# Performance work log

Measured on AMD Instinct MI355X. Metric: run time of the kernel, lower is better.

Reference implementation:

```python
import jax, jax.numpy as jnp
import numpy as np

B, N, E, H = 4, 4096, 1024, 16
D = E // H            # head_dim = 64
P_DIM = 64            # proj_dim; feature dim = 2*P_DIM = 128
EPS = 1e-4


def setup_inputs() -> dict:
    key = jax.random.key(0)
    ks = jax.random.split(key, 9)
    x = jax.random.normal(ks[0], (B, N, E), jnp.float32)
    init = 0.02
    Wq = jax.random.normal(ks[1], (E, E), jnp.float32) * init
    Wk = jax.random.normal(ks[2], (E, E), jnp.float32) * init
    Wv = jax.random.normal(ks[3], (E, E), jnp.float32) * init
    Wo = jax.random.normal(ks[4], (E, E), jnp.float32) * init
    bq = jnp.zeros((E,), jnp.float32)
    bk = jnp.zeros((E,), jnp.float32)
    bv = jnp.zeros((E,), jnp.float32)
    bo = jnp.zeros((E,), jnp.float32)
    # orthogonal random projection matrix (proj_dim, head_dim), fixed (non-trainable)
    g = np.random.default_rng(0).normal(size=(P_DIM, D))
    P = jnp.asarray(np.linalg.qr(g)[0], jnp.float32)
    return dict(x=x, Wq=Wq, bq=bq, Wk=Wk, bk=bk, Wv=Wv, bv=bv, Wo=Wo, bo=bo, P=P)


def _heads(z):
    # (B, N, E) -> (B, H, N, D)
    return z.reshape(B, N, H, D).transpose(0, 2, 1, 3)


def _normalize(z):
    return z / (jnp.linalg.norm(z, axis=-1, keepdims=True) + EPS)


def reference(x, Wq, bq, Wk, bk, Wv, bv, Wo, bo, P):
    q = _heads(x @ Wq.T + bq)
    k = _heads(x @ Wk.T + bk)
    v = _heads(x @ Wv.T + bv)
    q = _normalize(q)
    k = _normalize(k)
    scale = H ** 0.25
    qp = jnp.einsum('bhnd,ed->bhne', q, P) * scale
    kp = jnp.einsum('bhnd,ed->bhne', k, P) * scale
    fscale = P_DIM ** (-0.5)   # x.shape[-1]**-0.5 with last dim = proj_dim
    qf = jnp.concatenate([jnp.sin(qp), jnp.cos(qp)], axis=-1) * fscale  # (B,H,N,2p)
    kf = jnp.concatenate([jnp.sin(kp), jnp.cos(kp)], axis=-1) * fscale
    # non-causal linear attention: q @ (k^T v)
    kv = jnp.einsum('bhme,bhmd->bhed', kf, v)          # (B,H,2p,D)
    o = jnp.einsum('bhne,bhed->bhnd', qf, kv)          # (B,H,N,D)
    o = o.transpose(0, 2, 1, 3).reshape(B, N, E)
    return o @ Wo.T + bo
```

## Files before the change

kernel.cpp:

```cpp
#include <hip/hip_runtime.h>
#include <hip/hip_bf16.h>
#include <stdint.h>


typedef __bf16 bf16x8 __attribute__((ext_vector_type(8)));
typedef float f32x4 __attribute__((ext_vector_type(4)));

#define AS1 __attribute__((address_space(1)))
#define AS3 __attribute__((address_space(3)))

__device__ __forceinline__ void gl2lds16(const void* g, void* l) {
    __builtin_amdgcn_global_load_lds((const AS1 void*)g, (AS3 void*)l, 16, 0, 0);
}

static constexpr int GM = 16384, GN = 1024, GK = 1024;
static constexpr int KV_SLABS = 8;

__global__ void detect_kernel(const unsigned short* __restrict__ x,
                              int* __restrict__ flag) {
    __shared__ int s;
    const int lane = threadIdx.x;
    if (lane == 0) s = 0;
    __syncthreads();
    int cnt = 0;
#pragma unroll
    for (int i = 0; i < 2; ++i) {
        const unsigned short u = x[i * 64 + lane];
        const int e = (u >> 7) & 0xFF;
        cnt += (e >= 117 && e <= 131) ? 1 : 0;
    }
    atomicAdd(&s, cnt);
    __syncthreads();
    if (lane == 0) *flag = (s >= 100) ? 1 : 0;
}

__global__ __launch_bounds__(256) void cvt_kernel(
    const void* __restrict__ src, __hip_bfloat16* __restrict__ dst,
    int n, const int* __restrict__ flag) {
    if (*flag) return;
    const int i = (blockIdx.x * 256 + threadIdx.x) * 8;
    if (i >= n) return;
    const float* s = (const float*)src + i;
    const float4 a = *(const float4*)s;
    const float4 b = *(const float4*)(s + 4);
    union { uint4 u; __hip_bfloat16 h[8]; } pk;
    pk.h[0] = __float2bfloat16(a.x); pk.h[1] = __float2bfloat16(a.y);
    pk.h[2] = __float2bfloat16(a.z); pk.h[3] = __float2bfloat16(a.w);
    pk.h[4] = __float2bfloat16(b.x); pk.h[5] = __float2bfloat16(b.y);
    pk.h[6] = __float2bfloat16(b.z); pk.h[7] = __float2bfloat16(b.w);
    *(uint4*)(dst + i) = pk.u;
}

__global__ __launch_bounds__(512, 1) void gemm256_kernel(
    const void* __restrict__ Adirect,
    const __hip_bfloat16* __restrict__ Acvt,
    const void* __restrict__ Wr, const __hip_bfloat16* __restrict__ Wc,
    const void* __restrict__ bias_raw,
    void* __restrict__ Cout,
    const int* __restrict__ flag, int last)
{
    __shared__ unsigned short smem[65536];

    const int tid  = threadIdx.x;
    const int lane = tid & 63;
    const int w    = tid >> 6;
    const int wm   = w >> 2, wn = w & 3;
    const int lr   = lane & 15, lk = lane >> 4;

    const int id  = blockIdx.x;
    const int xcd = id & 7;
    const int s   = id >> 3;
    const int m0  = (xcd * 8 + (s >> 2)) * 256;
    const int n0  = (s & 3) * 256;
    const int fl  = *flag;

    const __hip_bfloat16* A = fl ? (const __hip_bfloat16*)Adirect : Acvt;
    const __hip_bfloat16* W = fl ? (const __hip_bfloat16*)Wr : Wc;
    const __hip_bfloat16* Ab = A + (size_t)m0 * GK;
    const __hip_bfloat16* Wb = W + (size_t)n0 * GK;

    f32x4 acc[8][4];
#pragma unroll
    for (int i = 0; i < 8; ++i)
#pragma unroll
        for (int j = 0; j < 4; ++j)
            acc[i][j] = (f32x4){0.f, 0.f, 0.f, 0.f};

    auto stage = [&](int p, int k0) {
        unsigned short* dA = smem + p * 32768;
        unsigned short* dB = dA + 16384;
#pragma unroll
        for (int j = 0; j < 4; ++j) {
            const int chunk = j * 512 + tid;
            const int row   = chunk >> 3;
            const int c     = chunk & 7;
            const int cs    = c ^ (row & 7);
            const size_t go = (size_t)row * GK + k0 + cs * 8;
            const int lo = (j * 512 + w * 64) * 16;
            gl2lds16(Ab + go, (char*)dA + lo);
            gl2lds16(Wb + go, (char*)dB + lo);
        }
    };

    auto compute = [&](int p) {
        const unsigned short* cA = smem + p * 32768;
        const unsigned short* cB = cA + 16384;
#pragma unroll
        for (int ks = 0; ks < 2; ++ks) {
            const int jj = (ks * 4 + lk) ^ (lr & 7);
            bf16x8 bfr[4];
#pragma unroll
            for (int j = 0; j < 4; ++j)
                bfr[j] = *(const bf16x8*)&cB[(wn * 64 + j * 16 + lr) * 64 + jj * 8];
            __builtin_amdgcn_s_setprio(1);
#pragma unroll
            for (int i = 0; i < 8; ++i) {
                const bf16x8 af =
                    *(const bf16x8*)&cA[(wm * 128 + i * 16 + lr) * 64 + jj * 8];
#pragma unroll
                for (int j = 0; j < 4; ++j)
                    acc[i][j] = __builtin_amdgcn_mfma_f32_16x16x32_bf16(
                        af, bfr[j], acc[i][j], 0, 0, 0);
            }
            __builtin_amdgcn_s_setprio(0);
        }
    };

    constexpr int NT = GK / 64;
    stage(0, 0);
    int p = 0;
    for (int kt = 0; kt < NT - 1; ++kt) {
        stage(p ^ 1, (kt + 1) * 64);
        asm volatile("s_waitcnt vmcnt(8)" ::: "memory");
        __builtin_amdgcn_s_barrier();
        compute(p);
        asm volatile("s_waitcnt lgkmcnt(0)" ::: "memory");
        __builtin_amdgcn_s_barrier();
        p ^= 1;
    }
    asm volatile("s_waitcnt vmcnt(0)" ::: "memory");
    __builtin_amdgcn_s_barrier();
    compute(p);
    asm volatile("s_waitcnt lgkmcnt(0)" ::: "memory");
    __builtin_amdgcn_s_barrier();

    const bool f32out = (last != 0) && (fl == 0);
    if (f32out) {
#pragma unroll
        for (int j = 0; j < 4; ++j) {
            const int col = n0 + wn * 64 + j * 16 + lr;
            const float bv = ((const float*)bias_raw)[col];
#pragma unroll
            for (int i = 0; i < 8; ++i) {
                const int rbase = m0 + wm * 128 + i * 16 + lk * 4;
#pragma unroll
                for (int r = 0; r < 4; ++r)
                    ((float*)Cout)[(size_t)(rbase + r) * GN + col] =
                        acc[i][j][r] + bv;
            }
        }
        return;
    }

    unsigned short* sC = smem;
#pragma unroll
    for (int j = 0; j < 4; ++j) {
        const int col = wn * 64 + j * 16 + lr;
        const float bv = fl ? __bfloat162float(((const __hip_bfloat16*)bias_raw)[n0 + col])
                            : ((const float*)bias_raw)[n0 + col];
        const int c_hi = col >> 3, off = col & 7;
#pragma unroll
        for (int i = 0; i < 8; ++i) {
            const int rb = wm * 128 + i * 16 + lk * 4;
#pragma unroll
            for (int r = 0; r < 4; ++r) {
                const int row = rb + r;
                const int phys = c_hi ^ (row & 7);
                __hip_bfloat16 hv = __float2bfloat16(acc[i][j][r] + bv);
                sC[row * 256 + phys * 8 + off] = *(unsigned short*)&hv;
            }
        }
    }
    __syncthreads();
    {
        const int row = tid >> 1, half = tid & 1;
        __hip_bfloat16* dst = (__hip_bfloat16*)Cout +
            (size_t)(m0 + row) * GN + n0 + half * 128;
#pragma unroll
        for (int q = 0; q < 16; ++q) {
            const int chunk = half * 16 + q;
            const int phys  = chunk ^ (row & 7);
            *(uint4*)(dst + q * 8) = *(const uint4*)&sC[row * 256 + phys * 8];
        }
    }
}

__device__ __forceinline__ void load_P(const void* Praw, int f,
                                       __hip_bfloat16* sP, int tid) {
    const int e = tid >> 2, q = tid & 3;
    union { uint4 u[2]; __hip_bfloat16 h[16]; } pk;
    if (f) {
        pk.u[0] = *(const uint4*)((const __hip_bfloat16*)Praw + e * 64 + q * 16);
        pk.u[1] = *(const uint4*)((const __hip_bfloat16*)Praw + e * 64 + q * 16 + 8);
    } else {
        const float* ps = (const float*)Praw + e * 64 + q * 16;
#pragma unroll
        for (int j = 0; j < 16; ++j) pk.h[j] = __float2bfloat16(ps[j]);
    }
    *(uint4*)&sP[e * 72 + q * 16]     = pk.u[0];
    *(uint4*)&sP[e * 72 + q * 16 + 8] = pk.u[1];
}

__device__ __forceinline__ float sumsq16(uint4 a, uint4 b) {
    union { uint4 u; __hip_bfloat16 h[8]; } x0, x1;
    x0.u = a; x1.u = b;
    float ss = 0.f;
#pragma unroll
    for (int j = 0; j < 8; ++j) {
        float v0 = __bfloat162float(x0.h[j]); ss += v0 * v0;
        float v1 = __bfloat162float(x1.h[j]); ss += v1 * v1;
    }
    return ss;
}

__global__ __launch_bounds__(256) void kv_kernel(
    const __hip_bfloat16* __restrict__ Km,
    const __hip_bfloat16* __restrict__ Vm,
    const void* __restrict__ Praw,
    float* __restrict__ PKV,
    const int* __restrict__ flag)
{
    __shared__ __hip_bfloat16 sK[64 * 72];
    __shared__ __hip_bfloat16 sVT[64 * 72];
    __shared__ __hip_bfloat16 sP[64 * 72];
    __shared__ __hip_bfloat16 sKFT[128 * 72];
    __shared__ float sRN[64];

    const int tid  = threadIdx.x;
    const int lane = tid & 63;
    const int w    = tid >> 6;
    const int lr   = lane & 15, lk = lane >> 4;
    const int bh   = blockIdx.y;
    const int b    = bh >> 4, h = bh & 15;
    const int nst  = blockIdx.x * 512;
    const int f    = *flag;
    const int n    = tid >> 2, q2 = tid & 3;

    load_P(Praw, f, sP, tid);

    f32x4 acck[2][4];
#pragma unroll
    for (int i = 0; i < 2; ++i)
#pragma unroll
        for (int j = 0; j < 4; ++j)
            acck[i][j] = (f32x4){0.f, 0.f, 0.f, 0.f};

    size_t base = ((size_t)(b * 4096 + nst + n)) * 1024 + h * 64 + q2 * 16;
    uint4 ka = *(const uint4*)(Km + base), kb = *(const uint4*)(Km + base + 8);
    uint4 va = *(const uint4*)(Vm + base), vb = *(const uint4*)(Vm + base + 8);

    for (int s = 0; s < 8; ++s) {
        __syncthreads();
        *(uint4*)&sK[n * 72 + q2 * 16]     = ka;
        *(uint4*)&sK[n * 72 + q2 * 16 + 8] = kb;
        {
            union { uint4 u[2]; __hip_bfloat16 h[16]; } vv;
            vv.u[0] = va; vv.u[1] = vb;
#pragma unroll
            for (int j = 0; j < 16; ++j) sVT[(q2 * 16 + j) * 72 + n] = vv.h[j];
        }
        {
            float ss = sumsq16(ka, kb);
            ss += __shfl_xor(ss, 1, 64);
            ss += __shfl_xor(ss, 2, 64);
            if (q2 == 0) sRN[n] = 2.0f / (sqrtf(ss) + 1e-4f);
        }
        if (s < 7) {
            base = ((size_t)(b * 4096 + nst + (s + 1) * 64 + n)) * 1024 + h * 64 + q2 * 16;
            ka = *(const uint4*)(Km + base); kb = *(const uint4*)(Km + base + 8);
            va = *(const uint4*)(Vm + base); vb = *(const uint4*)(Vm + base + 8);
        }
        {
            bf16x8 afr0 = *(const bf16x8*)&sK[(w * 16 + lr) * 72 + lk * 8];
            bf16x8 afr1 = *(const bf16x8*)&sK[(w * 16 + lr) * 72 + 32 + lk * 8];
            float rn[4];
#pragma unroll
            for (int r = 0; r < 4; ++r) rn[r] = sRN[w * 16 + lk * 4 + r];
#pragma unroll
            for (int eb = 0; eb < 4; ++eb) {
                f32x4 pa = (f32x4){0.f, 0.f, 0.f, 0.f};
                bf16x8 b0 = *(const bf16x8*)&sP[(eb * 16 + lr) * 72 + lk * 8];
                bf16x8 b1 = *(const bf16x8*)&sP[(eb * 16 + lr) * 72 + 32 + lk * 8];
                pa = __builtin_amdgcn_mfma_f32_16x16x32_bf16(afr0, b0, pa, 0, 0, 0);
                pa = __builtin_amdgcn_mfma_f32_16x16x32_bf16(afr1, b1, pa, 0, 0, 0);
                const int col = eb * 16 + lr;
#pragma unroll
                for (int r = 0; r < 4; ++r) {
                    const int row = w * 16 + lk * 4 + r;
                    float sv, cv;
                    __sincosf(pa[r] * rn[r], &sv, &cv);
                    sKFT[col * 72 + row]        = __float2bfloat16(sv * 0.125f);
                    sKFT[(col + 64) * 72 + row] = __float2bfloat16(cv * 0.125f);
                }
            }
        }
        __syncthreads();
#pragma unroll
        for (int ks = 0; ks < 2; ++ks) {
            bf16x8 a2[2], b2[4];
            a2[0] = *(const bf16x8*)&sKFT[(w * 16 + lr) * 72 + ks * 32 + lk * 8];
            a2[1] = *(const bf16x8*)&sKFT[((w + 4) * 16 + lr) * 72 + ks * 32 + lk * 8];
#pragma unroll
            for (int db = 0; db < 4; ++db)
                b2[db] = *(const bf16x8*)&sVT[(db * 16 + lr) * 72 + ks * 32 + lk * 8];
#pragma unroll
            for (int i = 0; i < 2; ++i)
#pragma unroll
                for (int db = 0; db < 4; ++db)
                    acck[i][db] = __builtin_amdgcn_mfma_f32_16x16x32_bf16(
                        a2[i], b2[db], acck[i][db], 0, 0, 0);
        }
    }

    float* out = PKV + ((size_t)blockIdx.x * 64 + bh) * 8192;
#pragma unroll
    for (int i = 0; i < 2; ++i)
#pragma unroll
        for (int db = 0; db < 4; ++db)
#pragma unroll
            for (int r = 0; r < 4; ++r) {
                const int e = (w + 4 * i) * 16 + lk * 4 + r;
                const int d = db * 16 + lr;
                out[e * 64 + d] = acck[i][db][r];
            }
}

__global__ __launch_bounds__(256) void kv_reduce_kernel(
    const float* __restrict__ PKV, float* __restrict__ gKV)
{
    const int i = (blockIdx.x * 256 + threadIdx.x) * 4;
    f32x4 s = (f32x4){0.f, 0.f, 0.f, 0.f};
#pragma unroll
    for (int sl = 0; sl < KV_SLABS; ++sl) {
        const float4 v = *(const float4*)(PKV + (size_t)sl * 64 * 8192 + i);
        s[0] += v.x; s[1] += v.y; s[2] += v.z; s[3] += v.w;
    }
    *(float4*)(gKV + i) = *(float4*)&s;
}

__global__ __launch_bounds__(256) void o_kernel(
    const __hip_bfloat16* __restrict__ Qm,
    const void* __restrict__ Praw,
    const float* __restrict__ gKV,
    __hip_bfloat16* __restrict__ O,
    const int* __restrict__ flag)
{
    __shared__ __hip_bfloat16 sQ[64 * 72];
    __shared__ __hip_bfloat16 sP[64 * 72];
    __shared__ __hip_bfloat16 sQF[64 * 136];
    __shared__ __hip_bfloat16 sKVT[64 * 136];
    __shared__ float sRN[64];

    const int tid  = threadIdx.x;
    const int lane = tid & 63;
    const int w    = tid >> 6;
    const int lr   = lane & 15, lk = lane >> 4;
    const int bh   = blockIdx.y;
    const int b    = bh >> 4, h = bh & 15;
    const int nst  = blockIdx.x * 256;
    const int f    = *flag;
    const int n    = tid >> 2, q2 = tid & 3;

    load_P(Praw, f, sP, tid);
    {
        const float* kvsrc = gKV + (size_t)bh * 8192;
        for (int t = tid; t < 8192; t += 256) {
            const int e = t >> 6, d = t & 63;
            sKVT[d * 136 + e] = __float2bfloat16(kvsrc[t]);
        }
    }

    size_t base = ((size_t)(b * 4096 + nst + n)) * 1024 + h * 64 + q2 * 16;
    uint4 qa = *(const uint4*)(Qm + base), qb = *(const uint4*)(Qm + base + 8);

    __syncthreads();

    for (int s = 0; s < 4; ++s) {
        const int gn0 = nst + s * 64;
        *(uint4*)&sQ[n * 72 + q2 * 16]     = qa;
        *(uint4*)&sQ[n * 72 + q2 * 16 + 8] = qb;
        {
            float ss = sumsq16(qa, qb);
            ss += __shfl_xor(ss, 1, 64);
            ss += __shfl_xor(ss, 2, 64);
            if (q2 == 0) sRN[n] = 2.0f / (sqrtf(ss) + 1e-4f);
        }
        if (s < 3) {
            base = ((size_t)(b * 4096 + nst + (s + 1) * 64 + n)) * 1024 + h * 64 + q2 * 16;
            qa = *(const uint4*)(Qm + base); qb = *(const uint4*)(Qm + base + 8);
        }
        {
            bf16x8 afr0 = *(const bf16x8*)&sQ[(w * 16 + lr) * 72 + lk * 8];
            bf16x8 afr1 = *(const bf16x8*)&sQ[(w * 16 + lr) * 72 + 32 + lk * 8];
            float rn[4];
#pragma unroll
            for (int r = 0; r < 4; ++r) rn[r] = sRN[w * 16 + lk * 4 + r];
#pragma unroll
            for (int eb = 0; eb < 4; ++eb) {
                f32x4 pa = (f32x4){0.f, 0.f, 0.f, 0.f};
                bf16x8 b0 = *(const bf16x8*)&sP[(eb * 16 + lr) * 72 + lk * 8];
                bf16x8 b1 = *(const bf16x8*)&sP[(eb * 16 + lr) * 72 + 32 + lk * 8];
                pa = __builtin_amdgcn_mfma_f32_16x16x32_bf16(afr0, b0, pa, 0, 0, 0);
                pa = __builtin_amdgcn_mfma_f32_16x16x32_bf16(afr1, b1, pa, 0, 0, 0);
                const int col = eb * 16 + lr;
#pragma unroll
                for (int r = 0; r < 4; ++r) {
                    const int row = w * 16 + lk * 4 + r;
                    float sv, cv;
                    __sincosf(pa[r] * rn[r], &sv, &cv);
                    sQF[row * 136 + col]      = __float2bfloat16(sv * 0.125f);
                    sQF[row * 136 + 64 + col] = __float2bfloat16(cv * 0.125f);
                }
            }
        }
        f32x4 oacc[4];
#pragma unroll
        for (int nb = 0; nb < 4; ++nb) oacc[nb] = (f32x4){0.f, 0.f, 0.f, 0.f};
#pragma unroll
        for (int ks = 0; ks < 4; ++ks) {
            bf16x8 aa = *(const bf16x8*)&sQF[(w * 16 + lr) * 136 + ks * 32 + lk * 8];
#pragma unroll
            for (int nb = 0; nb < 4; ++nb) {
                bf16x8 bb = *(const bf16x8*)&sKVT[(nb * 16 + lr) * 136 + ks * 32 + lk * 8];
                oacc[nb] = __builtin_amdgcn_mfma_f32_16x16x32_bf16(aa, bb, oacc[nb], 0, 0, 0);
            }
        }
#pragma unroll
        for (int nb = 0; nb < 4; ++nb)
#pragma unroll
            for (int r = 0; r < 4; ++r)
                sQ[(w * 16 + lk * 4 + r) * 72 + nb * 16 + lr] =
                    __float2bfloat16(oacc[nb][r]);
        {
            uint4 o0 = *(uint4*)&sQ[n * 72 + q2 * 16];
            uint4 o1 = *(uint4*)&sQ[n * 72 + q2 * 16 + 8];
            const size_t obase = ((size_t)(b * 4096 + gn0 + n)) * 1024 + h * 64 + q2 * 16;
            *(uint4*)(O + obase)     = o0;
            *(uint4*)(O + obase + 8) = o1;
        }
    }
}

extern "C" void kernel_launch(void* const* d_in, const int* in_sizes, int n_in,
                              void* d_out, int out_size, void* d_ws, size_t ws_size,
                              hipStream_t stream)
{
    (void)in_sizes; (void)n_in; (void)out_size; (void)ws_size;
    const void* x  = d_in[0];
    const void* Wq = d_in[1];
    const void* bq = d_in[2];
    const void* Wk = d_in[3];
    const void* bk = d_in[4];
    const void* Wv = d_in[5];
    const void* bv = d_in[6];
    const void* Wo = d_in[7];
    const void* bo = d_in[8];
    const void* P  = d_in[9];

    constexpr size_t XE = (size_t)GM * GN;
    constexpr size_t WE = (size_t)GN * GK;
    constexpr size_t KVE = (size_t)64 * 128 * 64;

    __hip_bfloat16* xb  = (__hip_bfloat16*)d_ws;
    __hip_bfloat16* wqb = xb + XE;
    __hip_bfloat16* wkb = wqb + WE;
    __hip_bfloat16* wvb = wkb + WE;
    __hip_bfloat16* wob = wvb + WE;
    __hip_bfloat16* R1  = wob + WE;
    __hip_bfloat16* R2  = R1 + XE;
    float* gKV = (float*)(R2 + XE);
    float* PKV = gKV + KVE;
    int* flag  = (int*)(PKV + (size_t)KV_SLABS * 64 * 8192);

    dim3 blk(256);
    hipLaunchKernelGGL(detect_kernel, dim3(1), dim3(64), 0, stream,
                       (const unsigned short*)x, flag);

    hipLaunchKernelGGL(cvt_kernel, dim3(8192), blk, 0, stream, x,  xb,  (int)XE, flag);
    hipLaunchKernelGGL(cvt_kernel, dim3(512),  blk, 0, stream, Wq, wqb, (int)WE, flag);
    hipLaunchKernelGGL(cvt_kernel, dim3(512),  blk, 0, stream, Wk, wkb, (int)WE, flag);
    hipLaunchKernelGGL(cvt_kernel, dim3(512),  blk, 0, stream, Wv, wvb, (int)WE, flag);
    hipLaunchKernelGGL(cvt_kernel, dim3(512),  blk, 0, stream, Wo, wob, (int)WE, flag);

    hipLaunchKernelGGL(gemm256_kernel, dim3(256), dim3(512), 0, stream,
                       x, xb, Wk, wkb, bk, R1, flag, 0);
    hipLaunchKernelGGL(gemm256_kernel, dim3(256), dim3(512), 0, stream,
                       x, xb, Wv, wvb, bv, R2, flag, 0);
    hipLaunchKernelGGL(kv_kernel, dim3(KV_SLABS, 64), blk, 0, stream, R1, R2, P, PKV, flag);
    hipLaunchKernelGGL(kv_reduce_kernel, dim3(512), blk, 0, stream, PKV, gKV);
    hipLaunchKernelGGL(gemm256_kernel, dim3(256), dim3(512), 0, stream,
                       x, xb, Wq, wqb, bq, R2, flag, 0);
    hipLaunchKernelGGL(o_kernel, dim3(16, 64), blk, 0, stream, R2, P, gKV, R1, flag);
    hipLaunchKernelGGL(gemm256_kernel, dim3(256), dim3(512), 0, stream,
                       R1, R1, Wo, wob, bo, d_out, flag, 1);
}
```

Measured before the change: 372.6 us.

## Rework GEMM main loop into 4-stage K=32 pipeline with split compute phases

Replaces the double-buffered K=64 loop with a four-slot ring of K=32 tiles, prefetching three tiles ahead and issuing each tile's global-to-LDS loads in two halves interleaved with two MFMA phases. LDS fragment offsets are precomputed and the swizzle is adapted to the 32-wide rows. Launch bounds are raised to request two blocks per CU. The aim is to hide global load latency and LDS reads behind MFMA work, at the cost of more barriers per K step and possible register pressure from the occupancy hint.

```diff
diff --git a/kernel.cpp b/kernel.cpp
--- a/kernel.cpp
+++ b/kernel.cpp
@@ -51,7 +51,7 @@
     *(uint4*)(dst + i) = pk.u;
 }
 
-__global__ __launch_bounds__(512, 1) void gemm256_kernel(
+__global__ __launch_bounds__(512, 2) void gemm256_kernel(
     const void* __restrict__ Adirect,
     const __hip_bfloat16* __restrict__ Acvt,
     const void* __restrict__ Wr, const __hip_bfloat16* __restrict__ Wc,
@@ -86,63 +86,88 @@
         for (int j = 0; j < 4; ++j)
             acc[i][j] = (f32x4){0.f, 0.f, 0.f, 0.f};
 
-    auto stage = [&](int p, int k0) {
-        unsigned short* dA = smem + p * 32768;
-        unsigned short* dB = dA + 16384;
-#pragma unroll
-        for (int j = 0; j < 4; ++j) {
-            const int chunk = j * 512 + tid;
-            const int row   = chunk >> 3;
-            const int c     = chunk & 7;
-            const int cs    = c ^ (row & 7);
-            const size_t go = (size_t)row * GK + k0 + cs * 8;
-            const int lo = (j * 512 + w * 64) * 16;
-            gl2lds16(Ab + go, (char*)dA + lo);
-            gl2lds16(Wb + go, (char*)dB + lo);
-        }
+    const int jj8 = (lk ^ ((lr >> 1) & 3)) * 8;
+    int offA[8], offB[4];
+#pragma unroll
+    for (int i = 0; i < 8; ++i)
+        offA[i] = (wm * 128 + i * 16 + lr) * 32 + jj8;
+#pragma unroll
+    for (int j = 0; j < 4; ++j)
+        offB[j] = 8192 + (wn * 64 + j * 16 + lr) * 32 + jj8;
+
+    size_t gofs[2];
+    int    ldso[2];
+#pragma unroll
+    for (int p = 0; p < 2; ++p) {
+        const int chunk = p * 512 + tid;
+        const int row   = chunk >> 2, c = chunk & 3;
+        const int cs    = c ^ ((row >> 1) & 3);
+        gofs[p] = (size_t)row * GK + cs * 8;
+        ldso[p] = (p * 512 + w * 64) * 16;
+    }
+
+    auto stage2 = [&](int t, int part) {
+        char* base = (char*)smem + (t & 3) * 32768 + ldso[part];
+        const size_t go = gofs[part] + (size_t)(t * 32);
+        gl2lds16(Ab + go, base);
+        gl2lds16(Wb + go, base + 16384);
     };
 
-    auto compute = [&](int p) {
-        const unsigned short* cA = smem + p * 32768;
-        const unsigned short* cB = cA + 16384;
-#pragma unroll
-        for (int ks = 0; ks < 2; ++ks) {
-            const int jj = (ks * 4 + lk) ^ (lr & 7);
-            bf16x8 bfr[4];
+    stage2(0, 0); stage2(0, 1);
+    stage2(1, 0); stage2(1, 1);
+    stage2(2, 0); stage2(2, 1);
+    asm volatile("s_waitcnt vmcnt(8)" ::: "memory");
+    __builtin_amdgcn_s_barrier();
+    __builtin_amdgcn_sched_barrier(0);
+
+    auto tile = [&](int t, bool do_stage, int gate) {
+        const unsigned short* sl = smem + (t & 3) * 16384;
+        bf16x8 af[4], bfr[4];
+#pragma unroll
+        for (int i = 0; i < 4; ++i) af[i] = *(const bf16x8*)&sl[offA[i]];
+#pragma unroll
+        for (int j = 0; j < 4; ++j) bfr[j] = *(const bf16x8*)&sl[offB[j]];
+        if (do_stage) stage2(t + 3, 0);
+        __builtin_amdgcn_s_barrier();
+        asm volatile("s_waitcnt lgkmcnt(0)" ::: "memory");
+        __builtin_amdgcn_sched_barrier(0);
+        __builtin_amdgcn_s_setprio(1);
+#pragma unroll
+        for (int i = 0; i < 4; ++i)
 #pragma unroll
             for (int j = 0; j < 4; ++j)
-                bfr[j] = *(const bf16x8*)&cB[(wn * 64 + j * 16 + lr) * 64 + jj * 8];
-            __builtin_amdgcn_s_setprio(1);
-#pragma unroll
-            for (int i = 0; i < 8; ++i) {
-                const bf16x8 af =
-                    *(const bf16x8*)&cA[(wm * 128 + i * 16 + lr) * 64 + jj * 8];
-#pragma unroll
-                for (int j = 0; j < 4; ++j)
-                    acc[i][j] = __builtin_amdgcn_mfma_f32_16x16x32_bf16(
-                        af, bfr[j], acc[i][j], 0, 0, 0);
-            }
-            __builtin_amdgcn_s_setprio(0);
-        }
+                acc[i][j] = __builtin_amdgcn_mfma_f32_16x16x32_bf16(
+                    af[i], bfr[j], acc[i][j], 0, 0, 0);
+        __builtin_amdgcn_s_setprio(0);
+        __builtin_amdgcn_s_barrier();
+        __builtin_amdgcn_sched_barrier(0);
+#pragma unroll
+        for (int i = 0; i < 4; ++i) af[i] = *(const bf16x8*)&sl[offA[4 + i]];
+        if (do_stage) stage2(t + 3, 1);
+        if (gate == 8)      asm volatile("s_waitcnt vmcnt(8)" ::: "memory");
+        else if (gate == 4) asm volatile("s_waitcnt vmcnt(4)" ::: "memory");
+        else                asm volatile("s_waitcnt vmcnt(0)" ::: "memory");
+        __builtin_amdgcn_s_barrier();
+        asm volatile("s_waitcnt lgkmcnt(0)" ::: "memory");
+        __builtin_amdgcn_sched_barrier(0);
+        __builtin_amdgcn_s_setprio(1);
+#pragma unroll
+        for (int i = 0; i < 4; ++i)
+#pragma unroll
+            for (int j = 0; j < 4; ++j)
+                acc[4 + i][j] = __builtin_amdgcn_mfma_f32_16x16x32_bf16(
+                    af[i], bfr[j], acc[4 + i][j], 0, 0, 0);
+        __builtin_amdgcn_s_setprio(0);
+        __builtin_amdgcn_s_barrier();
+        __builtin_amdgcn_sched_barrier(0);
     };
 
-    constexpr int NT = GK / 64;
-    stage(0, 0);
-    int p = 0;
-    for (int kt = 0; kt < NT - 1; ++kt) {
-        stage(p ^ 1, (kt + 1) * 64);
-        asm volatile("s_waitcnt vmcnt(8)" ::: "memory");
-        __builtin_amdgcn_s_barrier();
-        compute(p);
-        asm volatile("s_waitcnt lgkmcnt(0)" ::: "memory");
-        __builtin_amdgcn_s_barrier();
-        p ^= 1;
-    }
-    asm volatile("s_waitcnt vmcnt(0)" ::: "memory");
-    __builtin_amdgcn_s_barrier();
-    compute(p);
-    asm volatile("s_waitcnt lgkmcnt(0)" ::: "memory");
-    __builtin_amdgcn_s_barrier();
+    constexpr int NT = GK / 32;
+#pragma unroll 1
+    for (int t = 0; t < NT - 3; ++t) tile(t, true, 8);
+    tile(NT - 3, false, 4);
+    tile(NT - 2, false, 0);
+    tile(NT - 1, false, 0);
 
     const bool f32out = (last != 0) && (fl == 0);
     if (f32out) {
```

Result: no change. 375.2 us (+0.7%).
